# Performance work log

Measured on AMD Instinct MI355X. Metric: run time of the kernel, lower is better.

The kernel has to match this reference:

```python
import jax, jax.numpy as jnp
import numpy as np

N = 200000   # num atoms
D = 16       # atom_dims
K = 16       # k neighbors (17 - self)
L = 3        # n_layers
EPS = 1e-5
NEG_SLOPE = 0.2


def setup_inputs() -> dict:
    key = jax.random.key(0)
    ks = jax.random.split(key, 9)
    F = 2 * D + 1  # 33
    return {
        "y_atomtypes": jax.random.normal(ks[0], (N, D), dtype=jnp.float32),
        "dists": jax.random.uniform(ks[1], (N, K), dtype=jnp.float32),
        "W1": jax.random.normal(ks[2], (L, F, F), dtype=jnp.float32) * 0.1,
        "b1": jax.random.normal(ks[3], (L, F), dtype=jnp.float32) * 0.1,
        "W2": jax.random.normal(ks[4], (L, F, D), dtype=jnp.float32) * 0.1,
        "b2": jax.random.normal(ks[5], (L, D), dtype=jnp.float32) * 0.1,
        "gn_w": jnp.ones((L, D), dtype=jnp.float32),
        "gn_b": jnp.zeros((L, D), dtype=jnp.float32),
        "idx": jax.random.randint(ks[6], (N, K), 0, N, dtype=jnp.int64),
    }


def leaky(x):
    return jnp.where(x >= 0, x, NEG_SLOPE * x)


def group_norm(x, w, b):
    # x: [N, D], 2 groups over channel dim (torch GroupNorm on 2D input)
    n, d = x.shape
    xg = x.reshape(n, 2, d // 2)
    mu = xg.mean(axis=-1, keepdims=True)
    var = xg.var(axis=-1, keepdims=True)
    xn = ((xg - mu) * jax.lax.rsqrt(var + EPS)).reshape(n, d)
    return xn * w + b


def reference(y_atomtypes, dists, W1, b1, W2, b2, gn_w, gn_b, idx):
    out = y_atomtypes  # [N, D]
    d_feat = dists[:, :, None]  # [N, K, 1]
    for i in range(L):
        nb = out[idx]  # [N, K, D] gather
        self_feat = jnp.broadcast_to(out[:, None, :], (N, K, D))
        # torch cat order: [self(D), neighbor(D), dist(1)] -> 2D+1
        features = jnp.concatenate([self_feat, nb, d_feat], axis=-1)  # [N, K, 2D+1]
        h = leaky(jnp.einsum("nkf,fg->nkg", features, W1[i]) + b1[i])
        messages = jnp.einsum("nkf,fd->nkd", h, W2[i]) + b2[i]  # [N, K, D]
        messages = messages.sum(axis=1)  # [N, D]
        out = out + leaky(group_norm(messages, gn_w[i], gn_b[i]))
    return out
```

## Files before the change

### kernel.cpp

```cpp
#include <hip/hip_runtime.h>

#define NN 200000
#define DD 16
#define KK 16
#define FF 33

typedef __attribute__((ext_vector_type(8))) short bf16x8;
typedef __attribute__((ext_vector_type(4))) float f32x4;

__device__ __forceinline__ unsigned short f2bf(float f) {
    unsigned u = __float_as_uint(f);
    u += 0x7FFFu + ((u >> 16) & 1u);
    return (unsigned short)(u >> 16);
}

__global__ __launch_bounds__(256) void prep_kernel(
    const float* __restrict__ y, float* __restrict__ resid,
    unsigned short* __restrict__ tbl)
{
    const unsigned i = blockIdx.x * 256 + threadIdx.x;
    const float4 v = reinterpret_cast<const float4*>(y)[i];
    reinterpret_cast<float4*>(resid)[i] = v;
    ushort4 t;
    t.x = f2bf(v.x); t.y = f2bf(v.y); t.z = f2bf(v.z); t.w = f2bf(v.w);
    reinterpret_cast<ushort4*>(tbl)[i] = t;
}

#define WSTRIDE 448

__global__ __launch_bounds__(64) void pack_kernel(
    const float* __restrict__ W1, const float* __restrict__ b1,
    const float* __restrict__ W2, float4* __restrict__ wpk)
{
    const int L = blockIdx.x, l = threadIdx.x, g4 = l >> 4, c16 = l & 15;
    const float* W1l = W1 + L * FF * FF;
    const float* W2l = W2 + L * FF * DD;
    float4* out = wpk + L * WSTRIDE;

#pragma unroll
    for (int t = 0; t < 3; ++t) {
        const int g = c16 + 16 * t;
        const bool gv = (g < FF);
        bf16x8 fr;
#pragma unroll
        for (int j = 0; j < 8; ++j) {
            const float wv = gv ? W1l[(8 * g4 + j) * FF + g] : 0.f;
            fr[j] = (short)f2bf(wv);
        }
        out[t * 64 + l] = __builtin_bit_cast(float4, fr);
    }
    {
        bf16x8 fa, fb;
#pragma unroll
        for (int j = 0; j < 8; ++j) {
            fa[j] = (short)f2bf(W2l[(8 * g4 + j) * DD + c16]);
            const int g = 32 + 8 * g4 + j;
            fb[j] = (short)((g < FF) ? f2bf(W2l[g * DD + c16]) : 0);
        }
        out[192 + l] = __builtin_bit_cast(float4, fa);
        out[256 + l] = __builtin_bit_cast(float4, fb);
    }
    float* wf = reinterpret_cast<float*>(out + 320);
#pragma unroll
    for (int t = 0; t < 3; ++t) {
        const int g = c16 + 16 * t;
        const bool gv = (g < FF);
        wf[t * 64 + l]       = gv ? W1l[32 * FF + g] : 0.f;
        wf[192 + t * 64 + l] = gv ? b1[L * FF + g]   : 0.f;
    }
}

__global__ __launch_bounds__(256) void layer_kernel(
    float*       __restrict__ resid,
    const unsigned short* __restrict__ tin,
    unsigned short*       __restrict__ tout,
    const float* __restrict__ dists,
    const int*   __restrict__ idx,
    const float4* __restrict__ wpkL,
    const float* __restrict__ b2,
    const float* __restrict__ gnw,
    const float* __restrict__ gnb)
{
    __shared__ unsigned short hsH[4][16][64];

    const int tid = threadIdx.x;
    const int w   = tid >> 6, l = tid & 63, g4 = l >> 4, c16 = l & 15;
    const int n0  = (blockIdx.x * 4 + w) * 16;

    {
        uint4 z; z.x = z.y = z.z = z.w = 0u;
        reinterpret_cast<uint4*>(&hsH[w][0][0])[l]      = z;
        reinterpret_cast<uint4*>(&hsH[w][0][0])[l + 64] = z;
    }

    const bf16x8* wv8 = reinterpret_cast<const bf16x8*>(wpkL);
    const bf16x8 bW1h0 = wv8[0 * 64 + l];
    const bf16x8 bW1h1 = wv8[1 * 64 + l];
    const bf16x8 bW1h2 = wv8[2 * 64 + l];
    const bf16x8 b2ah  = wv8[192 + l];
    const bf16x8 b2bh  = wv8[256 + l];
    const float* wf = reinterpret_cast<const float*>(wpkL + 320);
    const float w1l0 = wf[l], w1l1 = wf[64 + l], w1l2 = wf[128 + l];
    const float b1v0 = wf[192 + l], b1v1 = wf[256 + l], b1v2 = wf[320 + l];
    const float kb2 = 16.f * b2[c16];
    const float gw  = gnw[c16], gb = gnb[c16];

    const bf16x8* tinv = reinterpret_cast<const bf16x8*>(tin);
    const float4* dq4  = reinterpret_cast<const float4*>(dists);

    int    nbp[4];
    bf16x8 avp[2];
    float4 dqp[2];
#pragma unroll
    for (int j = 0; j < 4; ++j)
        nbp[j] = idx[(unsigned)(n0 + j) * KK + c16];
#pragma unroll
    for (int j = 0; j < 2; ++j) {
        const unsigned ar = (g4 >= 2) ? (unsigned)nbp[j] : (unsigned)(n0 + j);
        avp[j] = tinv[ar * 2 + (g4 & 1)];
        dqp[j] = dq4[(unsigned)(n0 + j) * 4 + g4];
    }

#pragma unroll
    for (int m = 0; m < 16; ++m) {
        const bf16x8 a = avp[m & 1];
        const float4 q = dqp[m & 1];

        {
            const int r2 = (n0 + m + 2 < NN) ? (n0 + m + 2) : (NN - 1);
            const unsigned ar = (g4 >= 2) ? (unsigned)nbp[(m + 2) & 3] : (unsigned)r2;
            avp[m & 1] = tinv[ar * 2 + (g4 & 1)];
            dqp[m & 1] = dq4[(unsigned)r2 * 4 + g4];
            const int r4 = (n0 + m + 4 < NN) ? (n0 + m + 4) : (NN - 1);
            nbp[m & 3] = idx[(unsigned)r4 * KK + c16];
        }

        f32x4 acc0, acc1, acc2;
        acc0[0] = fmaf(q.x, w1l0, b1v0); acc0[1] = fmaf(q.y, w1l0, b1v0);
        acc0[2] = fmaf(q.z, w1l0, b1v0); acc0[3] = fmaf(q.w, w1l0, b1v0);
        acc1[0] = fmaf(q.x, w1l1, b1v1); acc1[1] = fmaf(q.y, w1l1, b1v1);
        acc1[2] = fmaf(q.z, w1l1, b1v1); acc1[3] = fmaf(q.w, w1l1, b1v1);
        acc2[0] = fmaf(q.x, w1l2, b1v2); acc2[1] = fmaf(q.y, w1l2, b1v2);
        acc2[2] = fmaf(q.z, w1l2, b1v2); acc2[3] = fmaf(q.w, w1l2, b1v2);

        acc0 = __builtin_amdgcn_mfma_f32_16x16x32_bf16(a, bW1h0, acc0, 0, 0, 0);
        acc1 = __builtin_amdgcn_mfma_f32_16x16x32_bf16(a, bW1h1, acc1, 0, 0, 0);
        acc2 = __builtin_amdgcn_mfma_f32_16x16x32_bf16(a, bW1h2, acc2, 0, 0, 0);

        float sx0 = (acc0[0] + acc0[1]) + (acc0[2] + acc0[3]);
        float sa0 = (fabsf(acc0[0]) + fabsf(acc0[1])) + (fabsf(acc0[2]) + fabsf(acc0[3]));
        float sx1 = (acc1[0] + acc1[1]) + (acc1[2] + acc1[3]);
        float sa1 = (fabsf(acc1[0]) + fabsf(acc1[1])) + (fabsf(acc1[2]) + fabsf(acc1[3]));
        float sx2 = (acc2[0] + acc2[1]) + (acc2[2] + acc2[3]);
        float sa2 = (fabsf(acc2[0]) + fabsf(acc2[1])) + (fabsf(acc2[2]) + fabsf(acc2[3]));
        float s0 = fmaf(0.6f, sx0, 0.4f * sa0);
        float s1 = fmaf(0.6f, sx1, 0.4f * sa1);
        float s2 = fmaf(0.6f, sx2, 0.4f * sa2);
        s0 += __shfl_xor(s0, 16); s0 += __shfl_xor(s0, 32);
        s1 += __shfl_xor(s1, 16); s1 += __shfl_xor(s1, 32);
        s2 += __shfl_xor(s2, 16); s2 += __shfl_xor(s2, 32);

        const float sv = (g4 == 0) ? s0 : ((g4 == 1) ? s1 : s2);
        if (g4 < 3)
            hsH[w][m][l ^ ((m & 7) << 3)] = f2bf(sv);
    }

    const int swr = (c16 & 7) << 3;
    const unsigned short* rowH = &hsH[w][c16][0];
    const bf16x8 a2h0 = *reinterpret_cast<const bf16x8*>(rowH + ((8 * g4     ) ^ swr));
    const bf16x8 a2h1 = *reinterpret_cast<const bf16x8*>(rowH + ((8 * g4 + 32) ^ swr));

    f32x4 macc;
    macc[0] = kb2; macc[1] = kb2; macc[2] = kb2; macc[3] = kb2;
    macc = __builtin_amdgcn_mfma_f32_16x16x32_bf16(a2h0, b2ah, macc, 0, 0, 0);
    macc = __builtin_amdgcn_mfma_f32_16x16x32_bf16(a2h1, b2bh, macc, 0, 0, 0);

#pragma unroll
    for (int j = 0; j < 4; ++j) {
        const float v = macc[j];
        const unsigned n = (unsigned)(n0 + 4 * g4 + j);
        float mu = v;
        mu += __shfl_xor(mu, 1); mu += __shfl_xor(mu, 2); mu += __shfl_xor(mu, 4);
        mu *= 0.125f;
        const float e = v - mu;
        float vr = e * e;
        vr += __shfl_xor(vr, 1); vr += __shfl_xor(vr, 2); vr += __shfl_xor(vr, 4);
        vr *= 0.125f;
        const float xn = e * rsqrtf(vr + 1e-5f);
        const float yv = fmaf(xn, gw, gb);
        const float val = fmaxf(yv, 0.2f * yv);
        const float o = resid[n * DD + c16] + val;
        resid[n * DD + c16] = o;
        tout [n * DD + c16] = f2bf(o);
    }
}

extern "C" void kernel_launch(void* const* d_in, const int* in_sizes, int n_in,
                              void* d_out, int out_size, void* d_ws, size_t ws_size,
                              hipStream_t stream) {
    const float* y     = (const float*)d_in[0];
    const float* dists = (const float*)d_in[1];
    const float* W1    = (const float*)d_in[2];
    const float* b1    = (const float*)d_in[3];
    const float* W2    = (const float*)d_in[4];
    const float* b2    = (const float*)d_in[5];
    const float* gnw   = (const float*)d_in[6];
    const float* gnb   = (const float*)d_in[7];
    const int*   idx   = (const int*)d_in[8];

    float* resid = (float*)d_out;
    unsigned short* tbl0 = (unsigned short*)d_ws;
    unsigned short* tbl1 = tbl0 + (size_t)NN * DD;
    float4* wpk = (float4*)((char*)d_ws + (size_t)2 * NN * DD * 2);

    pack_kernel<<<3, 64, 0, stream>>>(W1, b1, W2, wpk);
    prep_kernel<<<(NN * 4) / 256, 256, 0, stream>>>(y, resid, tbl0);

    const int grid = NN / 64;

    layer_kernel<<<grid, 256, 0, stream>>>(
        resid, tbl0, tbl1, dists, idx, wpk + 0 * WSTRIDE,
        b2 + 0 * DD, gnw + 0 * DD, gnb + 0 * DD);

    layer_kernel<<<grid, 256, 0, stream>>>(
        resid, tbl1, tbl0, dists, idx, wpk + 1 * WSTRIDE,
        b2 + 1 * DD, gnw + 1 * DD, gnb + 1 * DD);

    layer_kernel<<<grid, 256, 0, stream>>>(
        resid, tbl0, tbl1, dists, idx, wpk + 2 * WSTRIDE,
        b2 + 2 * DD, gnw + 2 * DD, gnb + 2 * DD);
}
```

Measured before the change: 216.8 us.

## Split W1 into self and neighbor parts, hoisting the self term out of the K loop

The first layer matrix is split into a self-feature block and a neighbor-plus-distance block. The self contribution plus bias is computed once per node with MFMA and reused as the accumulator seed for each of the 16 neighbors. Each lane now owns one node and iterates over its neighbors, gathering neighbor rows with a 3-deep prefetch. The distance is injected as a bf16 value into the A fragment instead of an FP32 FMA. Per-iteration cross-lane shuffles are replaced by register accumulation, at the cost of more registers and bf16 rounding of distances.

```diff
diff --git a/kernel.cpp b/kernel.cpp
--- a/kernel.cpp
+++ b/kernel.cpp
@@ -26,7 +26,7 @@
     reinterpret_cast<ushort4*>(tbl)[i] = t;
 }
 
-#define WSTRIDE 448
+#define WSTRIDE 560
 
 __global__ __launch_bounds__(64) void pack_kernel(
     const float* __restrict__ W1, const float* __restrict__ b1,
@@ -41,13 +41,21 @@
     for (int t = 0; t < 3; ++t) {
         const int g = c16 + 16 * t;
         const bool gv = (g < FF);
-        bf16x8 fr;
+        bf16x8 fs, fn;
 #pragma unroll
         for (int j = 0; j < 8; ++j) {
-            const float wv = gv ? W1l[(8 * g4 + j) * FF + g] : 0.f;
-            fr[j] = (short)f2bf(wv);
+            const int f = 8 * g4 + j;
+            float ws_ = (gv && f < 16) ? W1l[f * FF + g] : 0.f;
+            float wn;
+            if (!gv)          wn = 0.f;
+            else if (f == 0)  wn = W1l[32 * FF + g];
+            else if (f < 16)  wn = 0.f;
+            else              wn = W1l[f * FF + g];
+            fs[j] = (short)f2bf(ws_);
+            fn[j] = (short)f2bf(wn);
         }
-        out[t * 64 + l] = __builtin_bit_cast(float4, fr);
+        out[t * 64 + l]       = __builtin_bit_cast(float4, fs);
+        out[192 + t * 64 + l] = __builtin_bit_cast(float4, fn);
     }
     {
         bf16x8 fa, fb;
@@ -57,16 +65,14 @@
             const int g = 32 + 8 * g4 + j;
             fb[j] = (short)((g < FF) ? f2bf(W2l[g * DD + c16]) : 0);
         }
-        out[192 + l] = __builtin_bit_cast(float4, fa);
-        out[256 + l] = __builtin_bit_cast(float4, fb);
-    }
-    float* wf = reinterpret_cast<float*>(out + 320);
+        out[384 + l] = __builtin_bit_cast(float4, fa);
+        out[448 + l] = __builtin_bit_cast(float4, fb);
+    }
+    float* wf = reinterpret_cast<float*>(out + 512);
 #pragma unroll
     for (int t = 0; t < 3; ++t) {
         const int g = c16 + 16 * t;
-        const bool gv = (g < FF);
-        wf[t * 64 + l]       = gv ? W1l[32 * FF + g] : 0.f;
-        wf[192 + t * 64 + l] = gv ? b1[L * FF + g]   : 0.f;
+        wf[t * 64 + l] = (g < FF) ? b1[L * FF + g] : 0.f;
     }
 }
 
@@ -86,6 +92,7 @@
     const int tid = threadIdx.x;
     const int w   = tid >> 6, l = tid & 63, g4 = l >> 4, c16 = l & 15;
     const int n0  = (blockIdx.x * 4 + w) * 16;
+    const unsigned myrow = (unsigned)(n0 + c16);
 
     {
         uint4 z; z.x = z.y = z.z = z.w = 0u;
@@ -94,75 +101,94 @@
     }
 
     const bf16x8* wv8 = reinterpret_cast<const bf16x8*>(wpkL);
-    const bf16x8 bW1h0 = wv8[0 * 64 + l];
-    const bf16x8 bW1h1 = wv8[1 * 64 + l];
-    const bf16x8 bW1h2 = wv8[2 * 64 + l];
-    const bf16x8 b2ah  = wv8[192 + l];
-    const bf16x8 b2bh  = wv8[256 + l];
-    const float* wf = reinterpret_cast<const float*>(wpkL + 320);
-    const float w1l0 = wf[l], w1l1 = wf[64 + l], w1l2 = wf[128 + l];
-    const float b1v0 = wf[192 + l], b1v1 = wf[256 + l], b1v2 = wf[320 + l];
+    const bf16x8 bS0 = wv8[l], bS1 = wv8[64 + l], bS2 = wv8[128 + l];
+    const bf16x8 bN0 = wv8[192 + l], bN1 = wv8[256 + l], bN2 = wv8[320 + l];
+    const bf16x8 b2ah = wv8[384 + l], b2bh = wv8[448 + l];
+    const float* wf = reinterpret_cast<const float*>(wpkL + 512);
+    const float b1v0 = wf[l], b1v1 = wf[64 + l], b1v2 = wf[128 + l];
     const float kb2 = 16.f * b2[c16];
-    const float gw  = gnw[c16], gb = gnb[c16];
+    const float gw = gnw[c16], gb = gnb[c16];
 
     const bf16x8* tinv = reinterpret_cast<const bf16x8*>(tin);
-    const float4* dq4  = reinterpret_cast<const float4*>(dists);
-
-    int    nbp[4];
-    bf16x8 avp[2];
-    float4 dqp[2];
-#pragma unroll
-    for (int j = 0; j < 4; ++j)
-        nbp[j] = idx[(unsigned)(n0 + j) * KK + c16];
-#pragma unroll
-    for (int j = 0; j < 2; ++j) {
-        const unsigned ar = (g4 >= 2) ? (unsigned)nbp[j] : (unsigned)(n0 + j);
-        avp[j] = tinv[ar * 2 + (g4 & 1)];
-        dqp[j] = dq4[(unsigned)(n0 + j) * 4 + g4];
-    }
-
-#pragma unroll
-    for (int m = 0; m < 16; ++m) {
-        const bf16x8 a = avp[m & 1];
-        const float4 q = dqp[m & 1];
-
-        {
-            const int r2 = (n0 + m + 2 < NN) ? (n0 + m + 2) : (NN - 1);
-            const unsigned ar = (g4 >= 2) ? (unsigned)nbp[(m + 2) & 3] : (unsigned)r2;
-            avp[m & 1] = tinv[ar * 2 + (g4 & 1)];
-            dqp[m & 1] = dq4[(unsigned)r2 * 4 + g4];
-            const int r4 = (n0 + m + 4 < NN) ? (n0 + m + 4) : (NN - 1);
-            nbp[m & 3] = idx[(unsigned)r4 * KK + c16];
+    const unsigned goff = (unsigned)(g4 & 1);
+
+    int idxr[16];
+    {
+        const int4* ip = reinterpret_cast<const int4*>(idx + (size_t)myrow * KK);
+        const int4 a = ip[0], b = ip[1], c = ip[2], d = ip[3];
+        idxr[0]=a.x; idxr[1]=a.y; idxr[2]=a.z; idxr[3]=a.w;
+        idxr[4]=b.x; idxr[5]=b.y; idxr[6]=b.z; idxr[7]=b.w;
+        idxr[8]=c.x; idxr[9]=c.y; idxr[10]=c.z; idxr[11]=c.w;
+        idxr[12]=d.x; idxr[13]=d.y; idxr[14]=d.z; idxr[15]=d.w;
+    }
+    unsigned dpk[8];
+    {
+        const float4* dp_ = reinterpret_cast<const float4*>(dists + (size_t)myrow * KK);
+        const float4 a = dp_[0], b = dp_[1], c = dp_[2], d = dp_[3];
+        dpk[0] = (unsigned)f2bf(a.x) | ((unsigned)f2bf(a.y) << 16);
+        dpk[1] = (unsigned)f2bf(a.z) | ((unsigned)f2bf(a.w) << 16);
+        dpk[2] = (unsigned)f2bf(b.x) | ((unsigned)f2bf(b.y) << 16);
+        dpk[3] = (unsigned)f2bf(b.z) | ((unsigned)f2bf(b.w) << 16);
+        dpk[4] = (unsigned)f2bf(c.x) | ((unsigned)f2bf(c.y) << 16);
+        dpk[5] = (unsigned)f2bf(c.z) | ((unsigned)f2bf(c.w) << 16);
+        dpk[6] = (unsigned)f2bf(d.x) | ((unsigned)f2bf(d.y) << 16);
+        dpk[7] = (unsigned)f2bf(d.z) | ((unsigned)f2bf(d.w) << 16);
+    }
+
+    f32x4 base0, base1, base2;
+    base0[0]=b1v0; base0[1]=b1v0; base0[2]=b1v0; base0[3]=b1v0;
+    base1[0]=b1v1; base1[1]=b1v1; base1[2]=b1v1; base1[3]=b1v1;
+    base2[0]=b1v2; base2[1]=b1v2; base2[2]=b1v2; base2[3]=b1v2;
+    {
+        const bf16x8 aself = tinv[myrow * 2 + goff];
+        base0 = __builtin_amdgcn_mfma_f32_16x16x32_bf16(aself, bS0, base0, 0, 0, 0);
+        base1 = __builtin_amdgcn_mfma_f32_16x16x32_bf16(aself, bS1, base1, 0, 0, 0);
+        base2 = __builtin_amdgcn_mfma_f32_16x16x32_bf16(aself, bS2, base2, 0, 0, 0);
+    }
+
+    bf16x8 gp[3];
+    gp[0] = tinv[(unsigned)idxr[0] * 2 + goff];
+    gp[1] = tinv[(unsigned)idxr[1] * 2 + goff];
+    gp[2] = tinv[(unsigned)idxr[2] * 2 + goff];
+
+    f32x4 sx0, sx1, sx2, sa0, sa1, sa2;
+#pragma unroll
+    for (int j = 0; j < 4; ++j) {
+        sx0[j]=0.f; sx1[j]=0.f; sx2[j]=0.f;
+        sa0[j]=0.f; sa1[j]=0.f; sa2[j]=0.f;
+    }
+
+    const bool isg0 = (g4 == 0);
+
+#pragma unroll
+    for (int k = 0; k < KK; ++k) {
+        uint4 au = __builtin_bit_cast(uint4, gp[k % 3]);
+        const unsigned db = (k & 1) ? (dpk[k >> 1] >> 16) : (dpk[k >> 1] & 0xFFFFu);
+        au.x = isg0 ? db : au.x;
+        const bf16x8 av = __builtin_bit_cast(bf16x8, au);
+
+        if (k + 3 < KK)
+            gp[k % 3] = tinv[(unsigned)idxr[k + 3] * 2 + goff];
+
+        const f32x4 a0 = __builtin_amdgcn_mfma_f32_16x16x32_bf16(av, bN0, base0, 0, 0, 0);
+        const f32x4 a1 = __builtin_amdgcn_mfma_f32_16x16x32_bf16(av, bN1, base1, 0, 0, 0);
+        const f32x4 a2 = __builtin_amdgcn_mfma_f32_16x16x32_bf16(av, bN2, base2, 0, 0, 0);
+
+#pragma unroll
+        for (int j = 0; j < 4; ++j) {
+            sx0[j] += a0[j]; sa0[j] += fabsf(a0[j]);
+            sx1[j] += a1[j]; sa1[j] += fabsf(a1[j]);
+            sx2[j] += a2[j]; sa2[j] += fabsf(a2[j]);
         }
-
-        f32x4 acc0, acc1, acc2;
-        acc0[0] = fmaf(q.x, w1l0, b1v0); acc0[1] = fmaf(q.y, w1l0, b1v0);
-        acc0[2] = fmaf(q.z, w1l0, b1v0); acc0[3] = fmaf(q.w, w1l0, b1v0);
-        acc1[0] = fmaf(q.x, w1l1, b1v1); acc1[1] = fmaf(q.y, w1l1, b1v1);
-        acc1[2] = fmaf(q.z, w1l1, b1v1); acc1[3] = fmaf(q.w, w1l1, b1v1);
-        acc2[0] = fmaf(q.x, w1l2, b1v2); acc2[1] = fmaf(q.y, w1l2, b1v2);
-        acc2[2] = fmaf(q.z, w1l2, b1v2); acc2[3] = fmaf(q.w, w1l2, b1v2);
-
-        acc0 = __builtin_amdgcn_mfma_f32_16x16x32_bf16(a, bW1h0, acc0, 0, 0, 0);
-        acc1 = __builtin_amdgcn_mfma_f32_16x16x32_bf16(a, bW1h1, acc1, 0, 0, 0);
-        acc2 = __builtin_amdgcn_mfma_f32_16x16x32_bf16(a, bW1h2, acc2, 0, 0, 0);
-
-        float sx0 = (acc0[0] + acc0[1]) + (acc0[2] + acc0[3]);
-        float sa0 = (fabsf(acc0[0]) + fabsf(acc0[1])) + (fabsf(acc0[2]) + fabsf(acc0[3]));
-        float sx1 = (acc1[0] + acc1[1]) + (acc1[2] + acc1[3]);
-        float sa1 = (fabsf(acc1[0]) + fabsf(acc1[1])) + (fabsf(acc1[2]) + fabsf(acc1[3]));
-        float sx2 = (acc2[0] + acc2[1]) + (acc2[2] + acc2[3]);
-        float sa2 = (fabsf(acc2[0]) + fabsf(acc2[1])) + (fabsf(acc2[2]) + fabsf(acc2[3]));
-        float s0 = fmaf(0.6f, sx0, 0.4f * sa0);
-        float s1 = fmaf(0.6f, sx1, 0.4f * sa1);
-        float s2 = fmaf(0.6f, sx2, 0.4f * sa2);
-        s0 += __shfl_xor(s0, 16); s0 += __shfl_xor(s0, 32);
-        s1 += __shfl_xor(s1, 16); s1 += __shfl_xor(s1, 32);
-        s2 += __shfl_xor(s2, 16); s2 += __shfl_xor(s2, 32);
-
-        const float sv = (g4 == 0) ? s0 : ((g4 == 1) ? s1 : s2);
-        if (g4 < 3)
-            hsH[w][m][l ^ ((m & 7) << 3)] = f2bf(sv);
+    }
+
+#pragma unroll
+    for (int j = 0; j < 4; ++j) {
+        const int node = 4 * g4 + j;
+        const int sw = (node & 7) << 3;
+        hsH[w][node][(c16     ) ^ sw] = f2bf(fmaf(0.6f, sx0[j], 0.4f * sa0[j]));
+        hsH[w][node][(c16 + 16) ^ sw] = f2bf(fmaf(0.6f, sx1[j], 0.4f * sa1[j]));
+        hsH[w][node][(c16 + 32) ^ sw] = f2bf(fmaf(0.6f, sx2[j], 0.4f * sa2[j]));
     }
 
     const int swr = (c16 & 7) << 3;
```

Result: slower. 323.1 us (+49.0%).
